# Performance work log

Measured on AMD Instinct MI355X. Metric: run time of the kernel, lower is better.

Reference implementation:

```python
import jax, jax.numpy as jnp
import numpy as np
import math

B, L, IN_DIM, OUT_DIM = 2, 2048, 128, 128
H, DH = 8, 32            # num_heads, dim_head
ED = H * DH * 2          # embed_dim = 512
DEPTH = 1
LAMBDA_INIT = 0.8 - 0.6 * math.exp(-0.3 * (DEPTH + 1))
EPS = 1e-8


def setup_inputs() -> dict:
    key = jax.random.key(0)
    ks = jax.random.split(key, 10)
    x = jax.random.normal(ks[0], (B, 1, L, IN_DIM), dtype=jnp.float32)
    mask_2d = jax.random.bernoulli(ks[1], 0.9, (B, L, L))
    Wq = jax.random.normal(ks[2], (IN_DIM, ED), dtype=jnp.float32) * 0.05
    Wkv = jax.random.normal(ks[3], (IN_DIM, 2 * ED), dtype=jnp.float32) * 0.05
    Wout = jax.random.normal(ks[4], (ED, OUT_DIM), dtype=jnp.float32) * 0.05
    lambda_q1 = jax.random.normal(ks[5], (DH,), dtype=jnp.float32) * 0.1
    lambda_k1 = jax.random.normal(ks[6], (DH,), dtype=jnp.float32) * 0.1
    lambda_q2 = jax.random.normal(ks[7], (DH,), dtype=jnp.float32) * 0.1
    lambda_k2 = jax.random.normal(ks[8], (DH,), dtype=jnp.float32) * 0.1
    gamma = jnp.ones((2 * DH,), dtype=jnp.float32)
    return {"x": x, "mask_2d": mask_2d, "Wq": Wq, "Wkv": Wkv, "Wout": Wout,
            "lambda_q1": lambda_q1, "lambda_k1": lambda_k1,
            "lambda_q2": lambda_q2, "lambda_k2": lambda_k2, "gamma": gamma}


def reference(x, mask_2d, Wq, Wkv, Wout, lambda_q1, lambda_k1, lambda_q2, lambda_k2, gamma):
    b = x.shape[0]
    xs = x[:, 0]                                   # [b, L, in_dim]
    q = xs @ Wq                                    # [b, L, 2*H*DH]
    k, v = jnp.split(xs @ Wkv, 2, axis=-1)
    q = q.reshape(b, L, 2 * H, DH).transpose(0, 2, 1, 3) * (DH ** -0.5)  # [b,2H,L,d]
    k = k.reshape(b, L, 2 * H, DH).transpose(0, 2, 1, 3)                 # [b,2H,L,d]
    v = v.reshape(b, L, H, 2 * DH).transpose(0, 2, 1, 3)                 # [b,H,L,2d]
    dots = jnp.einsum('bnld,bnmd->bnlm', q, k)     # [b,2H,L,L]
    mask_value = -jnp.finfo(dots.dtype).max
    dots = jnp.where(mask_2d[:, None, :, :], dots, mask_value)
    attn_w = jax.nn.softmax(dots.astype(jnp.float32), axis=-1).astype(dots.dtype)
    lam1 = jnp.exp(jnp.sum(lambda_q1 * lambda_k1))
    lam2 = jnp.exp(jnp.sum(lambda_q2 * lambda_k2))
    lam = lam1 - lam2 + LAMBDA_INIT
    attn_w = attn_w.reshape(b, H, 2, L, L)
    attn_w = attn_w[:, :, 0] - lam * attn_w[:, :, 1]   # [b,H,L,L]
    attn = jnp.einsum('bhlm,bhmd->bhld', attn_w, v)    # [b,H,L,2d]
    rms = jnp.sqrt(jnp.mean(attn ** 2, axis=-1, keepdims=True))
    attn = gamma * (attn / (rms + EPS)) * (1.0 - LAMBDA_INIT)
    out = attn.transpose(0, 2, 1, 3).reshape(b, L, H * 2 * DH) @ Wout  # [b,L,out_dim]
    return out[:, None]                             # [b,1,L,out_dim]
```

## Files before the change

kernel.cpp:

```cpp
#include <hip/hip_runtime.h>
#include <float.h>
#include <math.h>

typedef __attribute__((ext_vector_type(8))) short short8;
typedef __attribute__((ext_vector_type(4))) float f32x4;

constexpr int SEQL = 2048;
constexpr int NQH  = 16;
constexpr int NVH  = 8;
constexpr int DHD  = 32;
constexpr float LAMB_INIT = 0.4707130183436648f;
constexpr float REPS      = 1e-8f;
constexpr float QW        = 0.25503492f;

static __device__ __forceinline__ unsigned short f2bf(float f) {
    union { float f; unsigned u; } a; a.f = f;
    unsigned u = a.u;
    u += 0x7fffu + ((u >> 16) & 1u);
    return (unsigned short)(u >> 16);
}

static __device__ __forceinline__ unsigned cvtpk(float lo, float hi) {
    unsigned r;
    asm("v_cvt_pk_bf16_f32 %0, %1, %2" : "=v"(r) : "v"(lo), "v"(hi));
    return r;
}

static __device__ __forceinline__ float expv(float x) {
    float r;
    asm("v_exp_f32 %0, %1" : "=v"(r) : "v"(x));
    return r;
}

static __device__ __forceinline__ void stage16(const unsigned short* g, unsigned short* l) {
    __builtin_amdgcn_global_load_lds(
        (const __attribute__((address_space(1))) unsigned int*)g,
        (__attribute__((address_space(3))) unsigned int*)l, 16, 0, 0);
}

__global__ __launch_bounds__(256) void wprep_kernel(
        const float* __restrict__ Wq, const float* __restrict__ Wkv,
        const float* __restrict__ Wout,
        unsigned short* __restrict__ Wf, unsigned short* __restrict__ WfO) {
    int gtid = blockIdx.x * 256 + threadIdx.x;
    #pragma unroll
    for (int i = 0; i < 4; ++i) {
        int e = gtid + i * 65536;
        int k = e >> 11, cc = e & 2047;
        if (cc < 1536) {
            float v = (cc < 512) ? Wq[(size_t)k * 512 + cc] * QW
                                 : Wkv[(size_t)k * 1024 + (cc - 512)];
            int cp = cc >> 4, lr = cc & 15, kk = k >> 5, lg = (k >> 3) & 3, j = k & 7;
            Wf[(((size_t)(cp * 4 + kk) * 4 + lg) * 16 + lr) * 8 + j] = f2bf(v);
        }
    }
    {
        int k = gtid >> 7, cc = gtid & 127;
        float v = Wout[gtid];
        int cp = cc >> 4, lr = cc & 15, kk = k >> 5, lg = (k >> 3) & 3, j = k & 7;
        WfO[(((size_t)(cp * 16 + kk) * 4 + lg) * 16 + lr) * 8 + j] = f2bf(v);
    }
}

__global__ __launch_bounds__(256) void qkv_mask_kernel(
        const float* __restrict__ x, const unsigned short* __restrict__ Wf,
        const unsigned char* __restrict__ mb, const int* __restrict__ mi,
        unsigned long long* __restrict__ bits,
        unsigned short* __restrict__ Q, unsigned short* __restrict__ Kf,
        unsigned short* __restrict__ Vf) {
    __shared__ int cnt[256];
    int t = threadIdx.x, w = t >> 6, lane = t & 63, lr = lane & 15, lg = lane >> 4;
    {
        int c = 0;
        #pragma unroll
        for (int i = 0; i < 16; ++i) c += (mb[t * 16 + i] != 0);
        cnt[t] = c;
    }
    __syncthreads();
    for (int s = 128; s > 0; s >>= 1) { if (t < s) cnt[t] += cnt[t + s]; __syncthreads(); }
    int f = cnt[0] > 2048;
    int lid = blockIdx.x;
    int swz = (lid & 7) * 192 + (lid >> 3);
    int by = swz >> 6, bx = swz & 63;
    int r0 = bx * 64 + w * 16;
    short8 ax[4];
    #pragma unroll
    for (int kk = 0; kk < 4; ++kk) {
        const float* xp = x + (size_t)(r0 + lr) * 128 + kk * 32 + lg * 8;
        float4 v0 = *(const float4*)xp;
        float4 v1 = *(const float4*)(xp + 4);
        union { short8 v; unsigned u[4]; } ua;
        ua.u[0] = cvtpk(v0.x, v0.y);
        ua.u[1] = cvtpk(v0.z, v0.w);
        ua.u[2] = cvtpk(v1.x, v1.y);
        ua.u[3] = cvtpk(v1.z, v1.w);
        ax[kk] = ua.v;
    }
    f32x4 acc[4];
    #pragma unroll
    for (int ct = 0; ct < 4; ++ct) acc[ct] = (f32x4){0.f, 0.f, 0.f, 0.f};
    #pragma unroll
    for (int ct = 0; ct < 4; ++ct) {
        int cp = by * 4 + ct;
        #pragma unroll
        for (int kk = 0; kk < 4; ++kk) {
            short8 bw = *(const short8*)(Wf + (size_t)(cp * 4 + kk) * 512 + lane * 8);
            acc[ct] = __builtin_amdgcn_mfma_f32_16x16x32_bf16(ax[kk], bw, acc[ct], 0, 0, 0);
        }
    }
    int gr0 = r0 + 4 * lg;
    int b = gr0 >> 11;
    if (by < 8) {
        #pragma unroll
        for (int ct = 0; ct < 4; ++ct) {
            int col = by * 64 + 16 * ct + lr;
            int n = col >> 5, d = col & 31;
            #pragma unroll
            for (int r = 0; r < 4; ++r) {
                int l = (gr0 + r) & 2047;
                Q[(((size_t)(b * NQH + n)) * SEQL + l) * DHD + d] = f2bf(acc[ct][r]);
            }
        }
    } else if (by < 16) {
        #pragma unroll
        for (int ct = 0; ct < 4; ++ct) {
            int ck = by * 64 + 16 * ct + lr - 512;
            int n = ck >> 5, dk = ck & 31;
            size_t hb = ((size_t)(b * NQH + n)) * 65536 + (dk >> 3) * 128 + (dk & 7);
            #pragma unroll
            for (int r = 0; r < 4; ++r) {
                int l = (gr0 + r) & 2047;
                Kf[hb + (size_t)((l >> 6) * 4 + ((l >> 4) & 3)) * 512 + (l & 15) * 8]
                    = f2bf(acc[ct][r]);
            }
        }
    } else {
        #pragma unroll
        for (int ct = 0; ct < 4; ++ct) {
            int cv = by * 64 + 16 * ct + lr - 1024;
            int h = cv >> 6, d = cv & 63;
            size_t hb = ((size_t)(b * NVH + h)) * 131072 + (d >> 4) * 512 + (d & 15) * 8;
            #pragma unroll
            for (int r = 0; r < 4; ++r) {
                int l = (gr0 + r) & 2047;
                Vf[hb + (size_t)((l >> 6) * 2 + ((l >> 5) & 1)) * 2048
                      + ((l >> 4) & 1) * 4 + ((l >> 2) & 3) * 128 + (l & 3)]
                    = f2bf(acc[ct][r]);
            }
        }
    }
    int wd0 = blockIdx.x * 4 + w;
    for (int wd = wd0; wd < 131072; wd += 6144) {
        int e = wd * 64 + lane;
        int v = f ? (int)mb[e] : mi[e];
        unsigned long long bl = __ballot(v != 0);
        if (lane == 0) bits[wd] = bl;
    }
}

__global__ __launch_bounds__(256, 2) void attn_kernel(
        const unsigned short* __restrict__ Q, const unsigned short* __restrict__ Kf,
        const unsigned short* __restrict__ Vf, const unsigned long long* __restrict__ bits,
        const float* __restrict__ lq1, const float* __restrict__ lk1,
        const float* __restrict__ lq2, const float* __restrict__ lk2,
        const float* __restrict__ gamma, unsigned short* __restrict__ A) {
    __shared__ unsigned short lds[4][8192];
    int tid = threadIdx.x;
    int w = tid >> 6, lane = tid & 63;
    int lr = lane & 15, lg = lane >> 4;
    int lid = blockIdx.y * 32 + blockIdx.x;
    int swz = (lid & 7) * 64 + (lid >> 3);
    int qtile = swz & 31, bh = swz >> 5;
    int b = bh >> 3, h = bh & 7;
    int q0 = qtile * 64 + w * 16;
    int bnA = b * NQH + 2 * h;

    short8 aqA = *(const short8*)(Q + (((size_t)bnA) * SEQL + q0 + lr) * DHD + lg * 8);
    short8 aqB = *(const short8*)(Q + (((size_t)(bnA + 1)) * SEQL + q0 + lr) * DHD + lg * 8);
    const unsigned short* KA = Kf + ((size_t)bnA) * 65536;
    const unsigned short* KB = KA + 65536;
    const unsigned short* VB = Vf + ((size_t)(b * NVH + h)) * 131072;
    const unsigned long long* mrow = bits + ((size_t)b * SEQL + q0 + lr) * 32;

    auto stage_tile = [&](int bf, int it) {
        #pragma unroll
        for (int j = 0; j < 4; ++j) {
            int c = 4 * w + j;
            const unsigned short* src =
                (c < 4) ? (KA + (size_t)it * 2048 + c * 512)
              : (c < 8) ? (KB + (size_t)it * 2048 + (c - 4) * 512)
                        : (VB + (size_t)it * 4096 + (c - 8) * 512);
            stage16(src + lane * 8, &lds[bf][c * 512]);
        }
    };

    f32x4 oA[4], oB[4];
    #pragma unroll
    for (int m = 0; m < 4; ++m) { oA[m] = (f32x4){0,0,0,0}; oB[m] = (f32x4){0,0,0,0}; }
    float ssA = 0.f, ssB = 0.f;
    unsigned long long mw = mrow[0];

    short8 paE[4], paO[4], bvE[8], bvO[8];
    #pragma unroll
    for (int i = 0; i < 4; ++i) { paE[i] = (short8){0,0,0,0,0,0,0,0}; paO[i] = (short8){0,0,0,0,0,0,0,0}; }
    #pragma unroll
    for (int i = 0; i < 8; ++i) { bvE[i] = (short8){0,0,0,0,0,0,0,0}; bvO[i] = (short8){0,0,0,0,0,0,0,0}; }

    stage_tile(0, 0);
    stage_tile(1, 1);

    auto body = [&](int t, short8* pa, short8* pbv, short8* npa, short8* nbv) {
        unsigned long long mwc = mw;
        mw = mrow[(t + 1) & 31];
        stage_tile((t + 2) & 3, (t + 2) & 31);
        asm volatile("s_waitcnt vmcnt(10)" ::: "memory");
        __builtin_amdgcn_s_barrier();
        __builtin_amdgcn_sched_barrier(0);
        const unsigned short* L = &lds[t & 3][0];
        short8 bkA[4], bkB[4];
        #pragma unroll
        for (int c = 0; c < 4; ++c) bkA[c] = *(const short8*)(L + c * 512 + lane * 8);
        #pragma unroll
        for (int c = 0; c < 4; ++c) bkB[c] = *(const short8*)(L + 2048 + c * 512 + lane * 8);
        #pragma unroll
        for (int z = 0; z < 8; ++z) nbv[z] = *(const short8*)(L + 4096 + z * 512 + lane * 8);
        f32x4 sA[4], sB[4];
        __builtin_amdgcn_s_setprio(1);
        #pragma unroll
        for (int c = 0; c < 4; ++c)
            sA[c] = __builtin_amdgcn_mfma_f32_16x16x32_bf16(bkA[c], aqA, (f32x4){0,0,0,0}, 0, 0, 0);
        #pragma unroll
        for (int c = 0; c < 4; ++c)
            sB[c] = __builtin_amdgcn_mfma_f32_16x16x32_bf16(bkB[c], aqB, (f32x4){0,0,0,0}, 0, 0, 0);
        #pragma unroll
        for (int m = 0; m < 4; ++m) {
            oA[m] = __builtin_amdgcn_mfma_f32_16x16x32_bf16(pa[0], pbv[m], oA[m], 0, 0, 0);
            oB[m] = __builtin_amdgcn_mfma_f32_16x16x32_bf16(pa[2], pbv[m], oB[m], 0, 0, 0);
        }
        #pragma unroll
        for (int m = 0; m < 4; ++m) {
            oA[m] = __builtin_amdgcn_mfma_f32_16x16x32_bf16(pa[1], pbv[4 + m], oA[m], 0, 0, 0);
            oB[m] = __builtin_amdgcn_mfma_f32_16x16x32_bf16(pa[3], pbv[4 + m], oB[m], 0, 0, 0);
        }
        __builtin_amdgcn_s_setprio(0);
        unsigned long long mwl = mwc >> (4 * lg);
        unsigned mlo = (unsigned)mwl, mhi = (unsigned)(mwl >> 32);
        float pA[4][4], pB[4][4];
        #pragma unroll
        for (int c = 0; c < 4; ++c) {
            unsigned wv = (c < 2) ? mlo : mhi;
            int sh = (c & 1) * 16;
            #pragma unroll
            for (int r = 0; r < 4; ++r) {
                unsigned keep = (wv >> (sh + r)) & 1u;
                float eA = expv(sA[c][r]);
                float eB = expv(sB[c][r]);
                pA[c][r] = keep ? eA : 0.f;
                pB[c][r] = keep ? eB : 0.f;
            }
        }
        float acA = 0.f, acB = 0.f;
        #pragma unroll
        for (int c = 0; c < 4; ++c)
            #pragma unroll
            for (int r = 0; r < 4; ++r) { acA += pA[c][r]; acB += pB[c][r]; }
        ssA += acA; ssB += acB;
        union { short8 v; unsigned u[4]; } a0, a1, b0, b1;
        a0.u[0] = cvtpk(pA[0][0], pA[0][1]); a0.u[1] = cvtpk(pA[0][2], pA[0][3]);
        a0.u[2] = cvtpk(pA[1][0], pA[1][1]); a0.u[3] = cvtpk(pA[1][2], pA[1][3]);
        a1.u[0] = cvtpk(pA[2][0], pA[2][1]); a1.u[1] = cvtpk(pA[2][2], pA[2][3]);
        a1.u[2] = cvtpk(pA[3][0], pA[3][1]); a1.u[3] = cvtpk(pA[3][2], pA[3][3]);
        b0.u[0] = cvtpk(pB[0][0], pB[0][1]); b0.u[1] = cvtpk(pB[0][2], pB[0][3]);
        b0.u[2] = cvtpk(pB[1][0], pB[1][1]); b0.u[3] = cvtpk(pB[1][2], pB[1][3]);
        b1.u[0] = cvtpk(pB[2][0], pB[2][1]); b1.u[1] = cvtpk(pB[2][2], pB[2][3]);
        b1.u[2] = cvtpk(pB[3][0], pB[3][1]); b1.u[3] = cvtpk(pB[3][2], pB[3][3]);
        npa[0] = a0.v; npa[1] = a1.v; npa[2] = b0.v; npa[3] = b1.v;
    };

    for (int tp = 0; tp < 16; ++tp) {
        body(2 * tp,     paE, bvE, paO, bvO);
        body(2 * tp + 1, paO, bvO, paE, bvE);
    }
    #pragma unroll
    for (int m = 0; m < 4; ++m) {
        oA[m] = __builtin_amdgcn_mfma_f32_16x16x32_bf16(paE[0], bvE[m], oA[m], 0, 0, 0);
        oB[m] = __builtin_amdgcn_mfma_f32_16x16x32_bf16(paE[2], bvE[m], oB[m], 0, 0, 0);
    }
    #pragma unroll
    for (int m = 0; m < 4; ++m) {
        oA[m] = __builtin_amdgcn_mfma_f32_16x16x32_bf16(paE[1], bvE[4 + m], oA[m], 0, 0, 0);
        oB[m] = __builtin_amdgcn_mfma_f32_16x16x32_bf16(paE[3], bvE[4 + m], oB[m], 0, 0, 0);
    }
    asm volatile("s_waitcnt vmcnt(0)" ::: "memory");
    ssA += __shfl_xor(ssA, 16, 64); ssA += __shfl_xor(ssA, 32, 64);
    ssB += __shfl_xor(ssB, 16, 64); ssB += __shfl_xor(ssB, 32, 64);
    float invA = 1.f / ssA, invB = 1.f / ssB;
    float iA[4], iB[4];
    #pragma unroll
    for (int r = 0; r < 4; ++r) {
        iA[r] = __shfl(invA, 4 * lg + r, 64);
        iB[r] = __shfl(invB, 4 * lg + r, 64);
    }
    int l31 = lane & 31;
    float t1 = lq1[l31] * lk1[l31];
    float t2 = lq2[l31] * lk2[l31];
    #pragma unroll
    for (int o = 1; o < 32; o <<= 1) { t1 += __shfl_xor(t1, o, 64); t2 += __shfl_xor(t2, o, 64); }
    float lam = __expf(t1) - __expf(t2) + LAMB_INIT;
    float dv[4][4];
    float sq[4] = {0.f, 0.f, 0.f, 0.f};
    #pragma unroll
    for (int m = 0; m < 4; ++m)
        #pragma unroll
        for (int r = 0; r < 4; ++r) {
            float v = oA[m][r] * iA[r] - lam * (oB[m][r] * iB[r]);
            dv[m][r] = v;
            sq[r] += v * v;
        }
    #pragma unroll
    for (int r = 0; r < 4; ++r) {
        #pragma unroll
        for (int o = 1; o < 16; o <<= 1) sq[r] += __shfl_xor(sq[r], o, 64);
        sq[r] = (1.f - LAMB_INIT) / (sqrtf(sq[r] * (1.f / 64.f)) + REPS);
    }
    float gm[4];
    #pragma unroll
    for (int m = 0; m < 4; ++m) gm[m] = gamma[16 * m + lr];
    unsigned short* Ab = A + ((size_t)(b * SEQL + q0 + 4 * lg)) * 512 + h * 64 + lr;
    #pragma unroll
    for (int m = 0; m < 4; ++m)
        #pragma unroll
        for (int r = 0; r < 4; ++r)
            Ab[(size_t)r * 512 + 16 * m] = f2bf(dv[m][r] * sq[r] * gm[m]);
}

__global__ __launch_bounds__(256) void proj_mfma_kernel(
        const unsigned short* __restrict__ Ab, const unsigned short* __restrict__ WfO,
        float* __restrict__ out) {
    __shared__ f32x4 red[1536];
    int t = threadIdx.x, w = t >> 6, lane = t & 63, lr = lane & 15, lg = lane >> 4;
    int r0 = blockIdx.x * 16;
    f32x4 acc[8];
    #pragma unroll
    for (int ct = 0; ct < 8; ++ct) acc[ct] = (f32x4){0.f, 0.f, 0.f, 0.f};
    #pragma unroll
    for (int j = 0; j < 4; ++j) {
        int kk = w * 4 + j;
        short8 af = *(const short8*)(Ab + (size_t)(r0 + lr) * 512 + kk * 32 + lg * 8);
        #pragma unroll
        for (int ct = 0; ct < 8; ++ct) {
            short8 bf = *(const short8*)(WfO + (size_t)(ct * 16 + kk) * 512 + lane * 8);
            acc[ct] = __builtin_amdgcn_mfma_f32_16x16x32_bf16(af, bf, acc[ct], 0, 0, 0);
        }
    }
    if (w) {
        #pragma unroll
        for (int ct = 0; ct < 8; ++ct)
            red[((w - 1) * 8 + ct) * 64 + lane] = acc[ct];
    }
    __syncthreads();
    if (w) return;
    #pragma unroll
    for (int ct = 0; ct < 8; ++ct) {
        #pragma unroll
        for (int j = 0; j < 3; ++j) {
            f32x4 pv = red[(j * 8 + ct) * 64 + lane];
            acc[ct][0] += pv[0]; acc[ct][1] += pv[1];
            acc[ct][2] += pv[2]; acc[ct][3] += pv[3];
        }
        #pragma unroll
        for (int r = 0; r < 4; ++r)
            out[(size_t)(r0 + 4 * lg + r) * 128 + ct * 16 + lr] = acc[ct][r];
    }
}

extern "C" void kernel_launch(void* const* d_in, const int* in_sizes, int n_in,
                              void* d_out, int out_size, void* d_ws, size_t ws_size,
                              hipStream_t stream) {
    const float* x    = (const float*)d_in[0];
    const void*  mask = d_in[1];
    const float* Wq   = (const float*)d_in[2];
    const float* Wkv  = (const float*)d_in[3];
    const float* Wout = (const float*)d_in[4];
    const float* lq1  = (const float*)d_in[5];
    const float* lk1  = (const float*)d_in[6];
    const float* lq2  = (const float*)d_in[7];
    const float* lk2  = (const float*)d_in[8];
    const float* gam  = (const float*)d_in[9];
    float* out = (float*)d_out;

    char* wsb = (char*)d_ws;
    unsigned long long* bits = (unsigned long long*)(wsb + 4096);
    unsigned short* Q        = (unsigned short*)(wsb + 1052672);
    unsigned short* Kf       = (unsigned short*)(wsb + 5246976);
    unsigned short* Vf       = (unsigned short*)(wsb + 9441280);
    unsigned short* Wf       = (unsigned short*)(wsb + 14684160);
    unsigned short* WfO      = (unsigned short*)(wsb + 15077376);
    unsigned short* Ab       = (unsigned short*)(wsb + 15208448);

    wprep_kernel<<<256, 256, 0, stream>>>(Wq, Wkv, Wout, Wf, WfO);
    qkv_mask_kernel<<<1536, 256, 0, stream>>>(x, Wf,
                                              (const unsigned char*)mask,
                                              (const int*)mask, bits, Q, Kf, Vf);
    attn_kernel<<<dim3(32, 16), 256, 0, stream>>>(Q, Kf, Vf, bits,
                                                  lq1, lk1, lq2, lk2, gam, Ab);
    proj_mfma_kernel<<<256, 256, 0, stream>>>(Ab, WfO, out);
}
```

Baseline: 90.99 us.

## Vectorize scattered stores via swapped MFMA operands and compute softmax sums with MFMA

Swaps the A/B operands of the MFMAs in the QKV and output projection kernels so each lane holds four consecutive columns. Scalar bf16 and float stores become packed uint2/float4 stores. The weight prep kernel now packs four k-values per thread. The attention kernel drops the per-tile scalar row-sum reduction and its cross-lane shuffles, and instead accumulates row sums with extra MFMAs against a ones vector. That adds matrix-core work and sums the bf16-rounded probabilities instead of the fp32 ones, which slightly changes numerics.

```diff
diff --git a/kernel.cpp b/kernel.cpp
--- a/kernel.cpp
+++ b/kernel.cpp
@@ -43,22 +43,28 @@
         const float* __restrict__ Wout,
         unsigned short* __restrict__ Wf, unsigned short* __restrict__ WfO) {
     int gtid = blockIdx.x * 256 + threadIdx.x;
-    #pragma unroll
-    for (int i = 0; i < 4; ++i) {
-        int e = gtid + i * 65536;
-        int k = e >> 11, cc = e & 2047;
-        if (cc < 1536) {
-            float v = (cc < 512) ? Wq[(size_t)k * 512 + cc] * QW
-                                 : Wkv[(size_t)k * 1024 + (cc - 512)];
-            int cp = cc >> 4, lr = cc & 15, kk = k >> 5, lg = (k >> 3) & 3, j = k & 7;
-            Wf[(((size_t)(cp * 4 + kk) * 4 + lg) * 16 + lr) * 8 + j] = f2bf(v);
-        }
-    }
-    {
-        int k = gtid >> 7, cc = gtid & 127;
-        float v = Wout[gtid];
-        int cp = cc >> 4, lr = cc & 15, kk = k >> 5, lg = (k >> 3) & 3, j = k & 7;
-        WfO[(((size_t)(cp * 16 + kk) * 4 + lg) * 16 + lr) * 8 + j] = f2bf(v);
+    if (gtid < 49152) {
+        int kq = gtid / 1536, cc = gtid - kq * 1536;
+        int k0 = kq * 4;
+        float v[4];
+        #pragma unroll
+        for (int i = 0; i < 4; ++i)
+            v[i] = (cc < 512) ? Wq[(size_t)(k0 + i) * 512 + cc] * QW
+                              : Wkv[(size_t)(k0 + i) * 1024 + (cc - 512)];
+        int cp = cc >> 4, lr = cc & 15, kk = k0 >> 5, lg = (k0 >> 3) & 3, j0 = k0 & 7;
+        uint2 pk;
+        pk.x = cvtpk(v[0], v[1]); pk.y = cvtpk(v[2], v[3]);
+        *(uint2*)(Wf + (((size_t)(cp * 4 + kk) * 4 + lg) * 16 + lr) * 8 + j0) = pk;
+    }
+    if (gtid < 16384) {
+        int cc = gtid & 127, k0 = (gtid >> 7) * 4;
+        float v[4];
+        #pragma unroll
+        for (int i = 0; i < 4; ++i) v[i] = Wout[(size_t)(k0 + i) * 128 + cc];
+        int cp = cc >> 4, lr = cc & 15, kk = k0 >> 5, lg = (k0 >> 3) & 3, j0 = k0 & 7;
+        uint2 pk;
+        pk.x = cvtpk(v[0], v[1]); pk.y = cvtpk(v[2], v[3]);
+        *(uint2*)(WfO + (((size_t)(cp * 16 + kk) * 4 + lg) * 16 + lr) * 8 + j0) = pk;
     }
 }
 
@@ -99,54 +105,60 @@
     f32x4 acc[4];
     #pragma unroll
     for (int ct = 0; ct < 4; ++ct) acc[ct] = (f32x4){0.f, 0.f, 0.f, 0.f};
-    #pragma unroll
-    for (int ct = 0; ct < 4; ++ct) {
-        int cp = by * 4 + ct;
-        #pragma unroll
-        for (int kk = 0; kk < 4; ++kk) {
-            short8 bw = *(const short8*)(Wf + (size_t)(cp * 4 + kk) * 512 + lane * 8);
-            acc[ct] = __builtin_amdgcn_mfma_f32_16x16x32_bf16(ax[kk], bw, acc[ct], 0, 0, 0);
-        }
-    }
-    int gr0 = r0 + 4 * lg;
-    int b = gr0 >> 11;
-    if (by < 8) {
-        #pragma unroll
-        for (int ct = 0; ct < 4; ++ct) {
-            int col = by * 64 + 16 * ct + lr;
-            int n = col >> 5, d = col & 31;
+    if (by < 16) {
+        #pragma unroll
+        for (int ct = 0; ct < 4; ++ct)
             #pragma unroll
-            for (int r = 0; r < 4; ++r) {
-                int l = (gr0 + r) & 2047;
-                Q[(((size_t)(b * NQH + n)) * SEQL + l) * DHD + d] = f2bf(acc[ct][r]);
+            for (int kk = 0; kk < 4; ++kk) {
+                short8 bw = *(const short8*)(Wf + (size_t)((by * 4 + ct) * 4 + kk) * 512 + lane * 8);
+                acc[ct] = __builtin_amdgcn_mfma_f32_16x16x32_bf16(bw, ax[kk], acc[ct], 0, 0, 0);
             }
-        }
-    } else if (by < 16) {
-        #pragma unroll
-        for (int ct = 0; ct < 4; ++ct) {
-            int ck = by * 64 + 16 * ct + lr - 512;
-            int n = ck >> 5, dk = ck & 31;
-            size_t hb = ((size_t)(b * NQH + n)) * 65536 + (dk >> 3) * 128 + (dk & 7);
+        int l = (r0 + lr) & 2047;
+        int b = (r0 + lr) >> 11;
+        if (by < 8) {
             #pragma unroll
-            for (int r = 0; r < 4; ++r) {
-                int l = (gr0 + r) & 2047;
-                Kf[hb + (size_t)((l >> 6) * 4 + ((l >> 4) & 3)) * 512 + (l & 15) * 8]
-                    = f2bf(acc[ct][r]);
+            for (int ct = 0; ct < 4; ++ct) {
+                int col = by * 64 + ct * 16 + 4 * lg;
+                int n = col >> 5, d = col & 31;
+                uint2 pk;
+                pk.x = cvtpk(acc[ct][0], acc[ct][1]);
+                pk.y = cvtpk(acc[ct][2], acc[ct][3]);
+                *(uint2*)(Q + (((size_t)(b * NQH + n)) * SEQL + l) * DHD + d) = pk;
             }
+        } else {
+            size_t lpart = (size_t)((l >> 6) * 4 + ((l >> 4) & 3)) * 512 + (l & 15) * 8;
+            #pragma unroll
+            for (int ct = 0; ct < 4; ++ct) {
+                int ck = by * 64 + ct * 16 + 4 * lg - 512;
+                int n = ck >> 5, dk = ck & 31;
+                uint2 pk;
+                pk.x = cvtpk(acc[ct][0], acc[ct][1]);
+                pk.y = cvtpk(acc[ct][2], acc[ct][3]);
+                *(uint2*)(Kf + ((size_t)(b * NQH + n)) * 65536 + lpart
+                             + (dk >> 3) * 128 + (dk & 7)) = pk;
+            }
         }
     } else {
+        #pragma unroll
+        for (int ct = 0; ct < 4; ++ct)
+            #pragma unroll
+            for (int kk = 0; kk < 4; ++kk) {
+                short8 bw = *(const short8*)(Wf + (size_t)((by * 4 + ct) * 4 + kk) * 512 + lane * 8);
+                acc[ct] = __builtin_amdgcn_mfma_f32_16x16x32_bf16(ax[kk], bw, acc[ct], 0, 0, 0);
+            }
+        int gr0 = r0 + 4 * lg;
+        int b = gr0 >> 11, l0 = gr0 & 2047;
+        size_t lpart = (size_t)((l0 >> 6) * 2 + ((l0 >> 5) & 1)) * 2048
+                     + ((l0 >> 4) & 1) * 4 + ((l0 >> 2) & 3) * 128;
         #pragma unroll
         for (int ct = 0; ct < 4; ++ct) {
             int cv = by * 64 + 16 * ct + lr - 1024;
             int h = cv >> 6, d = cv & 63;
-            size_t hb = ((size_t)(b * NVH + h)) * 131072 + (d >> 4) * 512 + (d & 15) * 8;
-            #pragma unroll
-            for (int r = 0; r < 4; ++r) {
-                int l = (gr0 + r) & 2047;
-                Vf[hb + (size_t)((l >> 6) * 2 + ((l >> 5) & 1)) * 2048
-                      + ((l >> 4) & 1) * 4 + ((l >> 2) & 3) * 128 + (l & 3)]
-                    = f2bf(acc[ct][r]);
-            }
+            uint2 pk;
+            pk.x = cvtpk(acc[ct][0], acc[ct][1]);
+            pk.y = cvtpk(acc[ct][2], acc[ct][3]);
+            *(uint2*)(Vf + ((size_t)(b * NVH + h)) * 131072
+                         + (size_t)(d >> 4) * 512 + (d & 15) * 8 + lpart) = pk;
         }
     }
     int wd0 = blockIdx.x * 4 + w;
@@ -182,6 +194,10 @@
     const unsigned short* VB = Vf + ((size_t)(b * NVH + h)) * 131072;
     const unsigned long long* mrow = bits + ((size_t)b * SEQL + q0 + lr) * 32;
 
+    short8 one8;
+    #pragma unroll
+    for (int i = 0; i < 8; ++i) one8[i] = (short)0x3F80;
+
     auto stage_tile = [&](int bf, int it) {
         #pragma unroll
         for (int j = 0; j < 4; ++j) {
@@ -194,10 +210,10 @@
         }
     };
 
-    f32x4 oA[4], oB[4];
+    f32x4 oA[4], oB[4], sumA, sumB;
     #pragma unroll
     for (int m = 0; m < 4; ++m) { oA[m] = (f32x4){0,0,0,0}; oB[m] = (f32x4){0,0,0,0}; }
-    float ssA = 0.f, ssB = 0.f;
+    sumA = (f32x4){0,0,0,0}; sumB = (f32x4){0,0,0,0};
     unsigned long long mw = mrow[0];
 
     short8 paE[4], paO[4], bvE[8], bvO[8];
@@ -259,12 +275,6 @@
                 pB[c][r] = keep ? eB : 0.f;
             }
         }
-        float acA = 0.f, acB = 0.f;
-        #pragma unroll
-        for (int c = 0; c < 4; ++c)
-            #pragma unroll
-            for (int r = 0; r < 4; ++r) { acA += pA[c][r]; acB += pB[c][r]; }
-        ssA += acA; ssB += acB;
         union { short8 v; unsigned u[4]; } a0, a1, b0, b1;
         a0.u[0] = cvtpk(pA[0][0], pA[0][1]); a0.u[1] = cvtpk(pA[0][2], pA[0][3]);
         a0.u[2] = cvtpk(pA[1][0], pA[1][1]); a0.u[3] = cvtpk(pA[1][2], pA[1][3]);
@@ -274,6 +284,10 @@
         b0.u[2] = cvtpk(pB[1][0], pB[1][1]); b0.u[3] = cvtpk(pB[1][2], pB[1][3]);
         b1.u[0] = cvtpk(pB[2][0], pB[2][1]); b1.u[1] = cvtpk(pB[2][2], pB[2][3]);
         b1.u[2] = cvtpk(pB[3][0], pB[3][1]); b1.u[3] = cvtpk(pB[3][2], pB[3][3]);
+        sumA = __builtin_amdgcn_mfma_f32_16x16x32_bf16(a0.v, one8, sumA, 0, 0, 0);
+        sumA = __builtin_amdgcn_mfma_f32_16x16x32_bf16(a1.v, one8, sumA, 0, 0, 0);
+        sumB = __builtin_amdgcn_mfma_f32_16x16x32_bf16(b0.v, one8, sumB, 0, 0, 0);
+        sumB = __builtin_amdgcn_mfma_f32_16x16x32_bf16(b1.v, one8, sumB, 0, 0, 0);
         npa[0] = a0.v; npa[1] = a1.v; npa[2] = b0.v; npa[3] = b1.v;
     };
 
@@ -292,14 +306,11 @@
         oB[m] = __builtin_amdgcn_mfma_f32_16x16x32_bf16(paE[3], bvE[4 + m], oB[m], 0, 0, 0);
     }
     asm volatile("s_waitcnt vmcnt(0)" ::: "memory");
-    ssA += __shfl_xor(ssA, 16, 64); ssA += __shfl_xor(ssA, 32, 64);
-    ssB += __shfl_xor(ssB, 16, 64); ssB += __shfl_xor(ssB, 32, 64);
-    float invA = 1.f / ssA, invB = 1.f / ssB;
     float iA[4], iB[4];
     #pragma unroll
     for (int r = 0; r < 4; ++r) {
-        iA[r] = __shfl(invA, 4 * lg + r, 64);
-        iB[r] = __shfl(invB, 4 * lg + r, 64);
+        iA[r] = 1.f / sumA[r];
+        iB[r] = 1.f / sumB[r];
     }
     int l31 = lane & 31;
     float t1 = lq1[l31] * lk1[l31];
@@ -350,7 +361,7 @@
         #pragma unroll
         for (int ct = 0; ct < 8; ++ct) {
             short8 bf = *(const short8*)(WfO + (size_t)(ct * 16 + kk) * 512 + lane * 8);
-            acc[ct] = __builtin_amdgcn_mfma_f32_16x16x32_bf16(af, bf, acc[ct], 0, 0, 0);
+            acc[ct] = __builtin_amdgcn_mfma_f32_16x16x32_bf16(bf, af, acc[ct], 0, 0, 0);
         }
     }
     if (w) {
@@ -368,9 +379,8 @@
             acc[ct][0] += pv[0]; acc[ct][1] += pv[1];
             acc[ct][2] += pv[2]; acc[ct][3] += pv[3];
         }
-        #pragma unroll
-        for (int r = 0; r < 4; ++r)
-            out[(size_t)(r0 + 4 * lg + r) * 128 + ct * 16 + lr] = acc[ct][r];
+        float4 st = { acc[ct][0], acc[ct][1], acc[ct][2], acc[ct][3] };
+        *(float4*)(out + (size_t)(r0 + lr) * 128 + ct * 16 + 4 * lg) = st;
     }
 }
 
```

Measured after the change: 86.88 us. 4.5% less time.
